# Performance work log

Measured on AMD Instinct MI355X. Metric: run time of the kernel, lower is better.

## Reference

```python
import jax, jax.numpy as jnp
import numpy as np

N_TOKENS, TOP_K, N_EXPERTS, HIDDEN, INTER = 4096, 2, 8, 1024, 2048


def setup_inputs() -> dict:
    key = jax.random.key(0)
    ks = jax.random.split(key, 6)
    std = float(np.sqrt(2.0 / (HIDDEN + INTER)))  # xavier-normal as in _init_weights
    tokens = jax.random.normal(ks[0], (N_TOKENS, HIDDEN), dtype=jnp.float32)
    expert_indices = jax.random.randint(ks[1], (N_TOKENS, TOP_K), 0, N_EXPERTS, dtype=jnp.int64)
    expert_weights = jax.random.uniform(ks[2], (N_TOKENS, TOP_K), dtype=jnp.float32)
    gate_weight = jax.random.normal(ks[3], (N_EXPERTS, HIDDEN, INTER), dtype=jnp.float32) * std
    up_weight = jax.random.normal(ks[4], (N_EXPERTS, HIDDEN, INTER), dtype=jnp.float32) * std
    down_weight = jax.random.normal(ks[5], (N_EXPERTS, INTER, HIDDEN), dtype=jnp.float32) * std
    return {"tokens": tokens, "expert_indices": expert_indices,
            "expert_weights": expert_weights, "gate_weight": gate_weight,
            "up_weight": up_weight, "down_weight": down_weight}


def reference(tokens, expert_indices, expert_weights, gate_weight, up_weight, down_weight):
    # Equivalent to the torch sort/group/scatter: since the expert output for a
    # token is independent of which top-k slot routed it, the combine reduces to
    # out[n] = sum_e cw[e, n] * FFN_e(tokens[n]), where cw[e, n] is the summed
    # routing weight of token n over slots whose index == e.
    n_experts = gate_weight.shape[0]
    onehot = jax.nn.one_hot(expert_indices, n_experts, dtype=tokens.dtype)  # [N,K,E]
    cw = jnp.einsum('nk,nke->en', expert_weights, onehot)  # [E,N] combine weights

    def body(acc, xs):
        g, u, d, w = xs  # g,u:[H,I]  d:[I,H]  w:[N]
        h = jax.nn.silu(tokens @ g) * (tokens @ u)  # [N,I] gated FFN hidden
        return acc + w[:, None] * (h @ d), None

    out0 = jnp.zeros_like(tokens)
    out, _ = jax.lax.scan(body, out0, (gate_weight, up_weight, down_weight, cw))
    return out
```

## Files before the change

### kernel.cpp

```cpp
#include <hip/hip_runtime.h>
#include <hip/hip_bf16.h>
#include <stdint.h>

#define NTOK  4096
#define TOPK  2
#define NEXP  8
#define HID   1024
#define INTER 2048
#define NPAIR (NTOK*TOPK)
#define MAXTILE 72

typedef __attribute__((ext_vector_type(8))) short short8;
typedef __attribute__((ext_vector_type(4))) float floatx4;

#define AS1(p) ((const __attribute__((address_space(1))) void*)(p))
#define AS3(p) ((__attribute__((address_space(3))) void*)(p))

#define O_PERMTOK 4096ull
#define O_PERMW   (O_PERMTOK + (size_t)NPAIR*4)
#define O_X       (1ull<<20)
#define O_WG      (O_X  + (size_t)NPAIR*HID*2)
#define O_WU      (O_WG + (size_t)NEXP*INTER*HID*2)
#define O_WD      (O_WU + (size_t)NEXP*INTER*HID*2)
#define O_HB      (O_WD + (size_t)NEXP*HID*INTER*2)
#define WS_NEEDED (O_HB + (size_t)NPAIR*INTER*2)

static __device__ __forceinline__ unsigned short f32_to_bf16_rne(float f) {
    union { float f; uint32_t u; } v; v.f = f;
    uint32_t b = v.u + 0x7fffu + ((v.u >> 16) & 1u);
    return (unsigned short)(b >> 16);
}
static __device__ __forceinline__ float bf16_to_f32(unsigned short u) {
    union { uint32_t i; float f; } cv; cv.i = ((uint32_t)u) << 16;
    return cv.f;
}

__global__ void k_probe(const void* __restrict__ tok, const void* __restrict__ ew,
                        const void* __restrict__ gw,  const void* __restrict__ uw,
                        const void* __restrict__ dw,  const void* __restrict__ eidx,
                        int* __restrict__ flags) {
    int lane = threadIdx.x;
    const void* ptrs[5] = { tok, ew, gw, uw, dw };
    for (int t = 0; t < 5; ++t) {
        const unsigned short* p = (const unsigned short*)ptrs[t];
        float v = bf16_to_f32(p[lane * 2]);
        unsigned long long m = __ballot(!(fabsf(v) < 1000.0f));
        if (lane == 0) flags[t] = (m != 0ull) ? 1 : 0;
    }
    const int* ix = (const int*)eidx;
    unsigned long long mi = __ballot(ix[lane * 2 + 1] != 0);
    if (lane == 0) flags[5] = (mi == 0ull) ? 1 : 0;
}

__global__ void k_route_count(const int* __restrict__ idx, int* __restrict__ counts,
                              const int* __restrict__ flags) {
    int i64 = flags[5];
    int p = blockIdx.x * 256 + threadIdx.x;
    if (p < NPAIR) atomicAdd(&counts[idx[p << i64]], 1);
}

__global__ void k_route_scan(const int* __restrict__ counts, int* __restrict__ offsets,
                             int* __restrict__ fill, int* __restrict__ ntiles,
                             int* __restrict__ tile_e, int* __restrict__ tile_m) {
    if (threadIdx.x == 0) {
        int acc = 0, nt = 0;
        for (int e = 0; e < NEXP; ++e) {
            offsets[e] = acc;
            for (int m = 0; m < counts[e]; m += 128) {
                tile_e[nt] = e; tile_m[nt] = m; ++nt;
            }
            acc += counts[e]; fill[e] = 0;
        }
        *ntiles = nt;
    }
}

__global__ void k_route_fill(const int* __restrict__ idx, const void* __restrict__ ew,
                             const int* __restrict__ offsets, int* __restrict__ fill,
                             int* __restrict__ perm_tok, float* __restrict__ perm_w,
                             const int* __restrict__ flags) {
    int ewf = flags[1], i64 = flags[5];
    int p = blockIdx.x * 256 + threadIdx.x;
    if (p < NPAIR) {
        int e = idx[p << i64];
        int pos = offsets[e] + atomicAdd(&fill[e], 1);
        perm_tok[pos] = p >> 1;
        perm_w[pos]   = ewf ? ((const float*)ew)[p]
                            : bf16_to_f32(((const unsigned short*)ew)[p]);
    }
}

__global__ void k_gather(const void* __restrict__ tokens, const int* __restrict__ perm_tok,
                         unsigned short* __restrict__ X, const int* __restrict__ flags) {
    int f = flags[0];
    int pos = blockIdx.x;
    int tok = perm_tok[pos];
    ushort4* d = (ushort4*)(X + (size_t)pos * HID);
    if (f) {
        float4 v = *(const float4*)((const float*)tokens + (size_t)tok * HID + threadIdx.x * 4);
        ushort4 o;
        o.x = f32_to_bf16_rne(v.x); o.y = f32_to_bf16_rne(v.y);
        o.z = f32_to_bf16_rne(v.z); o.w = f32_to_bf16_rne(v.w);
        d[threadIdx.x] = o;
    } else {
        d[threadIdx.x] = ((const ushort4*)((const unsigned short*)tokens + (size_t)tok * HID))[threadIdx.x];
    }
}

__global__ void k_transpose(const void* __restrict__ src,
                            unsigned short* __restrict__ dst, int R, int C,
                            const int* __restrict__ flags, int flagIdx) {
    __shared__ unsigned short tile[32][34];
    int isf32 = flags[flagIdx];
    size_t eoff = (size_t)blockIdx.z * R * C;
    const float* sf = (const float*)src + eoff;
    const unsigned short* sh = (const unsigned short*)src + eoff;
    dst += eoff;
    int c0 = blockIdx.x * 32, r0 = blockIdx.y * 32;
    int tx = threadIdx.x, ty = threadIdx.y;
#pragma unroll
    for (int i = 0; i < 32; i += 8) {
        size_t si = (size_t)(r0 + ty + i) * C + (c0 + tx);
        tile[ty + i][tx] = isf32 ? f32_to_bf16_rne(sf[si]) : sh[si];
    }
    __syncthreads();
#pragma unroll
    for (int i = 0; i < 32; i += 8)
        dst[(size_t)(c0 + ty + i) * R + (r0 + tx)] = tile[tx][ty + i];
}

__device__ __forceinline__ void stg16(const char* g, const unsigned short* ldsb) {
    __builtin_amdgcn_global_load_lds(AS1(g), AS3(ldsb), 16, 0, 0);
}

template<int KHW>
__device__ __forceinline__ void mfma_core(
    const unsigned short* __restrict__ Ab, int arowlim,
    const unsigned short* __restrict__ Bb,
    unsigned short* sA, unsigned short* sB,
    int tid, floatx4 (&acc)[4][4])
{
    const int wave = tid >> 6, lane = tid & 63;
    const int q = lane >> 4, l15 = lane & 15;
    const int wm = (wave >> 1) * 64, wn = (wave & 1) * 64;

    const int rl = lane >> 3;
    const int sch = (lane & 7) ^ (rl & 7);

    const char* gA[4]; const char* gB[4]; unsigned lb[4];
#pragma unroll
    for (int t = 0; t < 4; ++t) {
        int r = wave * 32 + t * 8 + rl;
        int ar = min(r, arowlim);
        gA[t] = (const char*)(Ab + (size_t)ar * KHW) + sch * 16;
        gB[t] = (const char*)(Bb + (size_t)r  * KHW) + sch * 16;
        lb[t] = (unsigned)((wave * 32 + t * 8) * 64);
    }

    const unsigned c0b = (unsigned)((q ^ (l15 & 7)) * 16);
    const char* cA = (const char*)sA;
    const char* cB = (const char*)sB;

#pragma unroll 1
    for (int kk = 0; kk < KHW / 64; ++kk) {
        const int kb = kk * 128;
#pragma unroll
        for (int t = 0; t < 4; ++t) stg16(gA[t] + kb, sA + lb[t]);
#pragma unroll
        for (int t = 0; t < 4; ++t) stg16(gB[t] + kb, sB + lb[t]);
        __syncthreads();
        short8 af[4][2], bfr[4][2];
#pragma unroll
        for (int i = 0; i < 4; ++i)
#pragma unroll
            for (int ks = 0; ks < 2; ++ks)
                af[i][ks] = *(const short8*)(cA + (wm + i * 16 + l15) * 128 + (c0b ^ (ks << 6)));
#pragma unroll
        for (int j = 0; j < 4; ++j)
#pragma unroll
            for (int ks = 0; ks < 2; ++ks)
                bfr[j][ks] = *(const short8*)(cB + (wn + j * 16 + l15) * 128 + (c0b ^ (ks << 6)));
#pragma unroll
        for (int i = 0; i < 4; ++i)
#pragma unroll
            for (int j = 0; j < 4; ++j) {
                acc[i][j] = __builtin_amdgcn_mfma_f32_16x16x32_bf16(af[i][0], bfr[j][0], acc[i][j], 0, 0, 0);
                acc[i][j] = __builtin_amdgcn_mfma_f32_16x16x32_bf16(af[i][1], bfr[j][1], acc[i][j], 0, 0, 0);
            }
        __syncthreads();
    }
}

template<int KHW>
__device__ __forceinline__ void mfma_core2(
    const unsigned short* __restrict__ Ab, int arowlim,
    const unsigned short* __restrict__ Bg, const unsigned short* __restrict__ Bu,
    unsigned short* sA, unsigned short* sBg, unsigned short* sBu,
    int tid, floatx4 (&accg)[4][4], floatx4 (&accu)[4][4])
{
    const int wave = tid >> 6, lane = tid & 63;
    const int q = lane >> 4, l15 = lane & 15;
    const int wm = (wave >> 1) * 64, wn = (wave & 1) * 64;

    const int rl = lane >> 3;
    const int sch = (lane & 7) ^ (rl & 7);

    const char* gA[4]; const char* gG[4]; const char* gU[4]; unsigned lb[4];
#pragma unroll
    for (int t = 0; t < 4; ++t) {
        int r = wave * 32 + t * 8 + rl;
        int ar = min(r, arowlim);
        gA[t] = (const char*)(Ab + (size_t)ar * KHW) + sch * 16;
        gG[t] = (const char*)(Bg + (size_t)r  * KHW) + sch * 16;
        gU[t] = (const char*)(Bu + (size_t)r  * KHW) + sch * 16;
        lb[t] = (unsigned)((wave * 32 + t * 8) * 64);
    }

    const unsigned c0b = (unsigned)((q ^ (l15 & 7)) * 16);
    const char* cA = (const char*)sA;
    const char* cG = (const char*)sBg;
    const char* cU = (const char*)sBu;

#pragma unroll 1
    for (int kk = 0; kk < KHW / 64; ++kk) {
        const int kb = kk * 128;
#pragma unroll
        for (int t = 0; t < 4; ++t) stg16(gA[t] + kb, sA + lb[t]);
#pragma unroll
        for (int t = 0; t < 4; ++t) stg16(gG[t] + kb, sBg + lb[t]);
#pragma unroll
        for (int t = 0; t < 4; ++t) stg16(gU[t] + kb, sBu + lb[t]);
        __syncthreads();
        short8 af[4][2];
#pragma unroll
        for (int i = 0; i < 4; ++i)
#pragma unroll
            for (int ks = 0; ks < 2; ++ks)
                af[i][ks] = *(const short8*)(cA + (wm + i * 16 + l15) * 128 + (c0b ^ (ks << 6)));
        {
            short8 b[4][2];
#pragma unroll
            for (int j = 0; j < 4; ++j)
#pragma unroll
                for (int ks = 0; ks < 2; ++ks)
                    b[j][ks] = *(const short8*)(cG + (wn + j * 16 + l15) * 128 + (c0b ^ (ks << 6)));
#pragma unroll
            for (int i = 0; i < 4; ++i)
#pragma unroll
                for (int j = 0; j < 4; ++j) {
                    accg[i][j] = __builtin_amdgcn_mfma_f32_16x16x32_bf16(af[i][0], b[j][0], accg[i][j], 0, 0, 0);
                    accg[i][j] = __builtin_amdgcn_mfma_f32_16x16x32_bf16(af[i][1], b[j][1], accg[i][j], 0, 0, 0);
                }
        }
        {
            short8 b[4][2];
#pragma unroll
            for (int j = 0; j < 4; ++j)
#pragma unroll
                for (int ks = 0; ks < 2; ++ks)
                    b[j][ks] = *(const short8*)(cU + (wn + j * 16 + l15) * 128 + (c0b ^ (ks << 6)));
#pragma unroll
            for (int i = 0; i < 4; ++i)
#pragma unroll
                for (int j = 0; j < 4; ++j) {
                    accu[i][j] = __builtin_amdgcn_mfma_f32_16x16x32_bf16(af[i][0], b[j][0], accu[i][j], 0, 0, 0);
                    accu[i][j] = __builtin_amdgcn_mfma_f32_16x16x32_bf16(af[i][1], b[j][1], accu[i][j], 0, 0, 0);
                }
        }
        __syncthreads();
    }
}

__global__ __launch_bounds__(256, 2) void k_gu(
    const unsigned short* __restrict__ X, const unsigned short* __restrict__ Wg,
    const unsigned short* __restrict__ Wu, unsigned short* __restrict__ Hbuf,
    const int* __restrict__ counts, const int* __restrict__ offsets,
    const int* __restrict__ tile_e, const int* __restrict__ tile_m,
    const int* __restrict__ ntiles)
{
    const int t = blockIdx.x;
    if (t >= *ntiles) return;
    const int e = tile_e[t], m0 = tile_m[t];
    const int cnt = counts[e], off = offsets[e];
    const int nt0 = blockIdx.y * 128;

    __shared__ __align__(16) unsigned short sA[128 * 64];
    __shared__ __align__(16) unsigned short sBg[128 * 64];
    __shared__ __align__(16) unsigned short sBu[128 * 64];

    const int tid = threadIdx.x;
    const int wave = tid >> 6, lane = tid & 63;
    const int wm = (wave >> 1) * 64, wn = (wave & 1) * 64;
    const int q = lane >> 4, l15 = lane & 15;

    floatx4 accg[4][4], accu[4][4];
#pragma unroll
    for (int i = 0; i < 4; ++i)
#pragma unroll
        for (int j = 0; j < 4; ++j)
#pragma unroll
            for (int r = 0; r < 4; ++r) { accg[i][j][r] = 0.f; accu[i][j][r] = 0.f; }

    mfma_core2<HID>(X + (size_t)(off + m0) * HID, NPAIR - 1 - (off + m0),
                    Wg + (size_t)e * INTER * HID + (size_t)nt0 * HID,
                    Wu + (size_t)e * INTER * HID + (size_t)nt0 * HID,
                    sA, sBg, sBu, tid, accg, accu);

#pragma unroll
    for (int i = 0; i < 4; ++i)
#pragma unroll
        for (int r = 0; r < 4; ++r) {
            int row = m0 + wm + i * 16 + q * 4 + r;
            if (row < cnt) {
                unsigned short* hrow = Hbuf + (size_t)(off + row) * INTER + nt0;
#pragma unroll
                for (int j = 0; j < 4; ++j) {
                    float g = accg[i][j][r];
                    float s = g / (1.0f + __expf(-g));
                    hrow[wn + j * 16 + l15] = f32_to_bf16_rne(s * accu[i][j][r]);
                }
            }
        }
}

__global__ __launch_bounds__(256) void k_d(
    const unsigned short* __restrict__ Hbuf, const unsigned short* __restrict__ Wd,
    float* __restrict__ outf,
    const int* __restrict__ counts, const int* __restrict__ offsets,
    const int* __restrict__ perm_tok, const float* __restrict__ perm_w,
    const int* __restrict__ tile_e, const int* __restrict__ tile_m,
    const int* __restrict__ ntiles)
{
    const int t = blockIdx.x;
    if (t >= *ntiles) return;
    const int e = tile_e[t], m0 = tile_m[t];
    const int cnt = counts[e], off = offsets[e];
    const int nt0 = blockIdx.y * 128;

    __shared__ __align__(16) unsigned short sA[128 * 64];
    __shared__ __align__(16) unsigned short sB[128 * 64];

    const int tid = threadIdx.x;
    const int wave = tid >> 6, lane = tid & 63;
    const int wm = (wave >> 1) * 64, wn = (wave & 1) * 64;
    const int q = lane >> 4, l15 = lane & 15;

    floatx4 acc[4][4];
#pragma unroll
    for (int i = 0; i < 4; ++i)
#pragma unroll
        for (int j = 0; j < 4; ++j)
#pragma unroll
            for (int r = 0; r < 4; ++r) acc[i][j][r] = 0.f;

    mfma_core<INTER>(Hbuf + (size_t)(off + m0) * INTER, NPAIR - 1 - (off + m0),
                     Wd + (size_t)e * HID * INTER + (size_t)nt0 * INTER, sA, sB, tid, acc);

#pragma unroll
    for (int i = 0; i < 4; ++i)
#pragma unroll
        for (int r = 0; r < 4; ++r) {
            int row = m0 + wm + i * 16 + q * 4 + r;
            if (row < cnt) {
                int gpos = off + row;
                int tok = perm_tok[gpos];
                float w = perm_w[gpos];
                float* orow = outf + (size_t)tok * HID + nt0;
#pragma unroll
                for (int j = 0; j < 4; ++j) {
#ifdef __HIP_PLATFORM_AMD__
                    unsafeAtomicAdd(&orow[wn + j * 16 + l15], w * acc[i][j][r]);
#else
                    atomicAdd(&orow[wn + j * 16 + l15], w * acc[i][j][r]);
#endif
                }
            }
        }
}

extern "C" void kernel_launch(void* const* d_in, const int* in_sizes, int n_in,
                              void* d_out, int out_size, void* d_ws, size_t ws_size,
                              hipStream_t stream) {
    const void* tokens = d_in[0];
    const void* eidx   = d_in[1];
    const void* ew     = d_in[2];
    const void* gw     = d_in[3];
    const void* uw     = d_in[4];
    const void* dwp    = d_in[5];
    float* out = (float*)d_out;
    char* ws = (char*)d_ws;

    if (ws_size < WS_NEEDED) {
        hipMemsetAsync(d_out, 0, (size_t)out_size * 4, stream);
        return;
    }

    int*   counts   = (int*)(ws + 0);
    int*   offsets  = (int*)(ws + 64);
    int*   fill     = (int*)(ws + 128);
    int*   flags    = (int*)(ws + 192);
    int*   ntiles   = (int*)(ws + 240);
    int*   tile_e   = (int*)(ws + 256);
    int*   tile_m   = (int*)(ws + 1024);
    int*   perm_tok = (int*)(ws + O_PERMTOK);
    float* perm_w   = (float*)(ws + O_PERMW);
    unsigned short* X  = (unsigned short*)(ws + O_X);
    unsigned short* Wg = (unsigned short*)(ws + O_WG);
    unsigned short* Wu = (unsigned short*)(ws + O_WU);
    unsigned short* Wd = (unsigned short*)(ws + O_WD);
    unsigned short* Hb = (unsigned short*)(ws + O_HB);

    hipMemsetAsync(counts, 0, 256, stream);
    hipMemsetAsync(out, 0, (size_t)out_size * 4, stream);

    k_probe<<<1, 64, 0, stream>>>(tokens, ew, gw, uw, dwp, eidx, flags);
    k_route_count<<<NPAIR / 256, 256, 0, stream>>>((const int*)eidx, counts, flags);
    k_route_scan<<<1, 64, 0, stream>>>(counts, offsets, fill, ntiles, tile_e, tile_m);
    k_route_fill<<<NPAIR / 256, 256, 0, stream>>>((const int*)eidx, ew, offsets, fill,
                                                  perm_tok, perm_w, flags);
    k_gather<<<NPAIR, 256, 0, stream>>>(tokens, perm_tok, X, flags);

    dim3 tb(32, 8);
    k_transpose<<<dim3(INTER / 32, HID / 32, NEXP), tb, 0, stream>>>(gw, Wg, HID, INTER, flags, 2);
    k_transpose<<<dim3(INTER / 32, HID / 32, NEXP), tb, 0, stream>>>(uw, Wu, HID, INTER, flags, 3);
    k_transpose<<<dim3(HID / 32, INTER / 32, NEXP), tb, 0, stream>>>(dwp, Wd, INTER, HID, flags, 4);

    k_gu<<<dim3(MAXTILE, INTER / 128), 256, 0, stream>>>(X, Wg, Wu, Hb, counts, offsets,
                                                         tile_e, tile_m, ntiles);
    k_d<<<dim3(MAXTILE, HID / 128), 256, 0, stream>>>(Hb, Wd, out, counts, offsets,
                                                      perm_tok, perm_w, tile_e, tile_m, ntiles);
}
```

Measured before the change: 541.7 us.

## Double-buffer LDS GEMM core, interleave gate/up weights, split-K down projection

Replaces the single-buffered MFMA loop with a double-buffered one that issues the global-to-LDS loads for the next K-tile while the current tile is computed. Gate and up weights are transposed into one interleaved matrix, so k_gu runs a single GEMM of twice the width and pairs the gate and up accumulators in the epilogue. k_d gains a split-K factor of 2 over INTER through blockIdx.z, relying on the existing atomic adds. The three transpose launches are merged into one. The trade-off is twice the LDS per block, which pressures occupancy, and more atomic traffic on the output.

```diff
diff --git a/kernel.cpp b/kernel.cpp
--- a/kernel.cpp
+++ b/kernel.cpp
@@ -19,11 +19,10 @@
 #define O_PERMTOK 4096ull
 #define O_PERMW   (O_PERMTOK + (size_t)NPAIR*4)
 #define O_X       (1ull<<20)
-#define O_WG      (O_X  + (size_t)NPAIR*HID*2)
-#define O_WU      (O_WG + (size_t)NEXP*INTER*HID*2)
-#define O_WD      (O_WU + (size_t)NEXP*INTER*HID*2)
-#define O_HB      (O_WD + (size_t)NEXP*HID*INTER*2)
-#define WS_NEEDED (O_HB + (size_t)NPAIR*INTER*2)
+#define O_WGU     (O_X   + (size_t)NPAIR*HID*2)
+#define O_WD      (O_WGU + (size_t)NEXP*2*INTER*HID*2)
+#define O_HB      (O_WD  + (size_t)NEXP*HID*INTER*2)
+#define WS_NEEDED (O_HB  + (size_t)NPAIR*INTER*2)
 
 static __device__ __forceinline__ unsigned short f32_to_bf16_rne(float f) {
     union { float f; uint32_t u; } v; v.f = f;
@@ -107,17 +106,26 @@
     }
 }
 
-__global__ void k_transpose(const void* __restrict__ src,
-                            unsigned short* __restrict__ dst, int R, int C,
-                            const int* __restrict__ flags, int flagIdx) {
+__global__ void k_transpose_all(const void* __restrict__ gw, const void* __restrict__ uw,
+                                const void* __restrict__ dwp,
+                                unsigned short* __restrict__ Wgu, unsigned short* __restrict__ Wd,
+                                const int* __restrict__ flags) {
     __shared__ unsigned short tile[32][34];
-    int isf32 = flags[flagIdx];
-    size_t eoff = (size_t)blockIdx.z * R * C;
+    const int z = blockIdx.y;
+    const int typ = z >> 3, e = z & 7;
+    const int R = (typ == 2) ? INTER : HID;
+    const int C = (typ == 2) ? HID : INTER;
+    const void* src = (typ == 0) ? gw : (typ == 1) ? uw : dwp;
+    const int isf32 = flags[2 + typ];
+    const size_t eoff = (size_t)e * HID * INTER;
     const float* sf = (const float*)src + eoff;
     const unsigned short* sh = (const unsigned short*)src + eoff;
-    dst += eoff;
-    int c0 = blockIdx.x * 32, r0 = blockIdx.y * 32;
-    int tx = threadIdx.x, ty = threadIdx.y;
+    unsigned short* dst = (typ == 2) ? (Wd + eoff) : (Wgu + (size_t)e * 2 * INTER * HID);
+
+    const int nbc = C / 32;
+    const int bx = blockIdx.x;
+    const int c0 = (bx % nbc) * 32, r0 = (bx / nbc) * 32;
+    const int tx = threadIdx.x, ty = threadIdx.y;
 #pragma unroll
     for (int i = 0; i < 32; i += 8) {
         size_t si = (size_t)(r0 + ty + i) * C + (c0 + tx);
@@ -125,16 +133,19 @@
     }
     __syncthreads();
 #pragma unroll
-    for (int i = 0; i < 32; i += 8)
-        dst[(size_t)(c0 + ty + i) * R + (r0 + tx)] = tile[tx][ty + i];
+    for (int i = 0; i < 32; i += 8) {
+        int c = c0 + ty + i;
+        int drow = (typ == 2) ? c : (((c >> 4) << 5) + (c & 15) + ((typ == 1) ? 16 : 0));
+        dst[(size_t)drow * R + (r0 + tx)] = tile[tx][ty + i];
+    }
 }
 
 __device__ __forceinline__ void stg16(const char* g, const unsigned short* ldsb) {
     __builtin_amdgcn_global_load_lds(AS1(g), AS3(ldsb), 16, 0, 0);
 }
 
-template<int KHW>
-__device__ __forceinline__ void mfma_core(
+template<int KHW, int NKT>
+__device__ __forceinline__ void coreK(
     const unsigned short* __restrict__ Ab, int arowlim,
     const unsigned short* __restrict__ Bb,
     unsigned short* sA, unsigned short* sB,
@@ -161,25 +172,35 @@
     const char* cA = (const char*)sA;
     const char* cB = (const char*)sB;
 
+#pragma unroll
+    for (int t = 0; t < 4; ++t) stg16(gA[t], sA + lb[t]);
+#pragma unroll
+    for (int t = 0; t < 4; ++t) stg16(gB[t], sB + lb[t]);
+    __syncthreads();
+
 #pragma unroll 1
-    for (int kk = 0; kk < KHW / 64; ++kk) {
-        const int kb = kk * 128;
-#pragma unroll
-        for (int t = 0; t < 4; ++t) stg16(gA[t] + kb, sA + lb[t]);
-#pragma unroll
-        for (int t = 0; t < 4; ++t) stg16(gB[t] + kb, sB + lb[t]);
-        __syncthreads();
+    for (int kt = 0; kt < NKT; ++kt) {
+        const int cur = kt & 1;
+        const unsigned curb = (unsigned)cur * 16384u;
+        if (kt + 1 < NKT) {
+            const int kb = (kt + 1) * 128;
+            const unsigned nxtb = (unsigned)(cur ^ 1) * 8192u;
+#pragma unroll
+            for (int t = 0; t < 4; ++t) stg16(gA[t] + kb, sA + nxtb + lb[t]);
+#pragma unroll
+            for (int t = 0; t < 4; ++t) stg16(gB[t] + kb, sB + nxtb + lb[t]);
+        }
         short8 af[4][2], bfr[4][2];
 #pragma unroll
         for (int i = 0; i < 4; ++i)
 #pragma unroll
             for (int ks = 0; ks < 2; ++ks)
-                af[i][ks] = *(const short8*)(cA + (wm + i * 16 + l15) * 128 + (c0b ^ (ks << 6)));
+                af[i][ks] = *(const short8*)(cA + curb + (wm + i * 16 + l15) * 128 + (c0b ^ (ks << 6)));
 #pragma unroll
         for (int j = 0; j < 4; ++j)
 #pragma unroll
             for (int ks = 0; ks < 2; ++ks)
-                bfr[j][ks] = *(const short8*)(cB + (wn + j * 16 + l15) * 128 + (c0b ^ (ks << 6)));
+                bfr[j][ks] = *(const short8*)(cB + curb + (wn + j * 16 + l15) * 128 + (c0b ^ (ks << 6)));
 #pragma unroll
         for (int i = 0; i < 4; ++i)
 #pragma unroll
@@ -191,89 +212,9 @@
     }
 }
 
-template<int KHW>
-__device__ __forceinline__ void mfma_core2(
-    const unsigned short* __restrict__ Ab, int arowlim,
-    const unsigned short* __restrict__ Bg, const unsigned short* __restrict__ Bu,
-    unsigned short* sA, unsigned short* sBg, unsigned short* sBu,
-    int tid, floatx4 (&accg)[4][4], floatx4 (&accu)[4][4])
-{
-    const int wave = tid >> 6, lane = tid & 63;
-    const int q = lane >> 4, l15 = lane & 15;
-    const int wm = (wave >> 1) * 64, wn = (wave & 1) * 64;
-
-    const int rl = lane >> 3;
-    const int sch = (lane & 7) ^ (rl & 7);
-
-    const char* gA[4]; const char* gG[4]; const char* gU[4]; unsigned lb[4];
-#pragma unroll
-    for (int t = 0; t < 4; ++t) {
-        int r = wave * 32 + t * 8 + rl;
-        int ar = min(r, arowlim);
-        gA[t] = (const char*)(Ab + (size_t)ar * KHW) + sch * 16;
-        gG[t] = (const char*)(Bg + (size_t)r  * KHW) + sch * 16;
-        gU[t] = (const char*)(Bu + (size_t)r  * KHW) + sch * 16;
-        lb[t] = (unsigned)((wave * 32 + t * 8) * 64);
-    }
-
-    const unsigned c0b = (unsigned)((q ^ (l15 & 7)) * 16);
-    const char* cA = (const char*)sA;
-    const char* cG = (const char*)sBg;
-    const char* cU = (const char*)sBu;
-
-#pragma unroll 1
-    for (int kk = 0; kk < KHW / 64; ++kk) {
-        const int kb = kk * 128;
-#pragma unroll
-        for (int t = 0; t < 4; ++t) stg16(gA[t] + kb, sA + lb[t]);
-#pragma unroll
-        for (int t = 0; t < 4; ++t) stg16(gG[t] + kb, sBg + lb[t]);
-#pragma unroll
-        for (int t = 0; t < 4; ++t) stg16(gU[t] + kb, sBu + lb[t]);
-        __syncthreads();
-        short8 af[4][2];
-#pragma unroll
-        for (int i = 0; i < 4; ++i)
-#pragma unroll
-            for (int ks = 0; ks < 2; ++ks)
-                af[i][ks] = *(const short8*)(cA + (wm + i * 16 + l15) * 128 + (c0b ^ (ks << 6)));
-        {
-            short8 b[4][2];
-#pragma unroll
-            for (int j = 0; j < 4; ++j)
-#pragma unroll
-                for (int ks = 0; ks < 2; ++ks)
-                    b[j][ks] = *(const short8*)(cG + (wn + j * 16 + l15) * 128 + (c0b ^ (ks << 6)));
-#pragma unroll
-            for (int i = 0; i < 4; ++i)
-#pragma unroll
-                for (int j = 0; j < 4; ++j) {
-                    accg[i][j] = __builtin_amdgcn_mfma_f32_16x16x32_bf16(af[i][0], b[j][0], accg[i][j], 0, 0, 0);
-                    accg[i][j] = __builtin_amdgcn_mfma_f32_16x16x32_bf16(af[i][1], b[j][1], accg[i][j], 0, 0, 0);
-                }
-        }
-        {
-            short8 b[4][2];
-#pragma unroll
-            for (int j = 0; j < 4; ++j)
-#pragma unroll
-                for (int ks = 0; ks < 2; ++ks)
-                    b[j][ks] = *(const short8*)(cU + (wn + j * 16 + l15) * 128 + (c0b ^ (ks << 6)));
-#pragma unroll
-            for (int i = 0; i < 4; ++i)
-#pragma unroll
-                for (int j = 0; j < 4; ++j) {
-                    accu[i][j] = __builtin_amdgcn_mfma_f32_16x16x32_bf16(af[i][0], b[j][0], accu[i][j], 0, 0, 0);
-                    accu[i][j] = __builtin_amdgcn_mfma_f32_16x16x32_bf16(af[i][1], b[j][1], accu[i][j], 0, 0, 0);
-                }
-        }
-        __syncthreads();
-    }
-}
-
 __global__ __launch_bounds__(256, 2) void k_gu(
-    const unsigned short* __restrict__ X, const unsigned short* __restrict__ Wg,
-    const unsigned short* __restrict__ Wu, unsigned short* __restrict__ Hbuf,
+    const unsigned short* __restrict__ X, const unsigned short* __restrict__ Wgu,
+    unsigned short* __restrict__ Hbuf,
     const int* __restrict__ counts, const int* __restrict__ offsets,
     const int* __restrict__ tile_e, const int* __restrict__ tile_m,
     const int* __restrict__ ntiles)
@@ -284,27 +225,25 @@
     const int cnt = counts[e], off = offsets[e];
     const int nt0 = blockIdx.y * 128;
 
-    __shared__ __align__(16) unsigned short sA[128 * 64];
-    __shared__ __align__(16) unsigned short sBg[128 * 64];
-    __shared__ __align__(16) unsigned short sBu[128 * 64];
+    __shared__ __align__(16) unsigned short sA[2 * 128 * 64];
+    __shared__ __align__(16) unsigned short sB[2 * 128 * 64];
 
     const int tid = threadIdx.x;
     const int wave = tid >> 6, lane = tid & 63;
     const int wm = (wave >> 1) * 64, wn = (wave & 1) * 64;
     const int q = lane >> 4, l15 = lane & 15;
 
-    floatx4 accg[4][4], accu[4][4];
+    floatx4 acc[4][4];
 #pragma unroll
     for (int i = 0; i < 4; ++i)
 #pragma unroll
         for (int j = 0; j < 4; ++j)
 #pragma unroll
-            for (int r = 0; r < 4; ++r) { accg[i][j][r] = 0.f; accu[i][j][r] = 0.f; }
-
-    mfma_core2<HID>(X + (size_t)(off + m0) * HID, NPAIR - 1 - (off + m0),
-                    Wg + (size_t)e * INTER * HID + (size_t)nt0 * HID,
-                    Wu + (size_t)e * INTER * HID + (size_t)nt0 * HID,
-                    sA, sBg, sBu, tid, accg, accu);
+            for (int r = 0; r < 4; ++r) acc[i][j][r] = 0.f;
+
+    coreK<HID, HID / 64>(X + (size_t)(off + m0) * HID, NPAIR - 1 - (off + m0),
+                         Wgu + (size_t)e * 2 * INTER * HID + (size_t)nt0 * HID,
+                         sA, sB, tid, acc);
 
 #pragma unroll
     for (int i = 0; i < 4; ++i)
@@ -312,18 +251,20 @@
         for (int r = 0; r < 4; ++r) {
             int row = m0 + wm + i * 16 + q * 4 + r;
             if (row < cnt) {
-                unsigned short* hrow = Hbuf + (size_t)(off + row) * INTER + nt0;
-#pragma unroll
-                for (int j = 0; j < 4; ++j) {
-                    float g = accg[i][j][r];
+                unsigned short* hrow = Hbuf + (size_t)(off + row) * INTER;
+#pragma unroll
+                for (int jp = 0; jp < 2; ++jp) {
+                    int j = jp * 2;
+                    float g = acc[i][j][r], u = acc[i][j + 1][r];
                     float s = g / (1.0f + __expf(-g));
-                    hrow[wn + j * 16 + l15] = f32_to_bf16_rne(s * accu[i][j][r]);
+                    int icol = (nt0 + wn) / 2 + jp * 16 + l15;
+                    hrow[icol] = f32_to_bf16_rne(s * u);
                 }
             }
         }
 }
 
-__global__ __launch_bounds__(256) void k_d(
+__global__ __launch_bounds__(256, 2) void k_d(
     const unsigned short* __restrict__ Hbuf, const unsigned short* __restrict__ Wd,
     float* __restrict__ outf,
     const int* __restrict__ counts, const int* __restrict__ offsets,
@@ -336,9 +277,10 @@
     const int e = tile_e[t], m0 = tile_m[t];
     const int cnt = counts[e], off = offsets[e];
     const int nt0 = blockIdx.y * 128;
-
-    __shared__ __align__(16) unsigned short sA[128 * 64];
-    __shared__ __align__(16) unsigned short sB[128 * 64];
+    const int z = blockIdx.z;
+
+    __shared__ __align__(16) unsigned short sA[2 * 128 * 64];
+    __shared__ __align__(16) unsigned short sB[2 * 128 * 64];
 
     const int tid = threadIdx.x;
     const int wave = tid >> 6, lane = tid & 63;
@@ -353,8 +295,9 @@
 #pragma unroll
             for (int r = 0; r < 4; ++r) acc[i][j][r] = 0.f;
 
-    mfma_core<INTER>(Hbuf + (size_t)(off + m0) * INTER, NPAIR - 1 - (off + m0),
-                     Wd + (size_t)e * HID * INTER + (size_t)nt0 * INTER, sA, sB, tid, acc);
+    coreK<INTER, 16>(Hbuf + (size_t)(off + m0) * INTER + z * 1024, NPAIR - 1 - (off + m0),
+                     Wd + (size_t)e * HID * INTER + (size_t)nt0 * INTER + z * 1024,
+                     sA, sB, tid, acc);
 
 #pragma unroll
     for (int i = 0; i < 4; ++i)
@@ -404,11 +347,10 @@
     int*   tile_m   = (int*)(ws + 1024);
     int*   perm_tok = (int*)(ws + O_PERMTOK);
     float* perm_w   = (float*)(ws + O_PERMW);
-    unsigned short* X  = (unsigned short*)(ws + O_X);
-    unsigned short* Wg = (unsigned short*)(ws + O_WG);
-    unsigned short* Wu = (unsigned short*)(ws + O_WU);
-    unsigned short* Wd = (unsigned short*)(ws + O_WD);
-    unsigned short* Hb = (unsigned short*)(ws + O_HB);
+    unsigned short* X   = (unsigned short*)(ws + O_X);
+    unsigned short* Wgu = (unsigned short*)(ws + O_WGU);
+    unsigned short* Wd  = (unsigned short*)(ws + O_WD);
+    unsigned short* Hb  = (unsigned short*)(ws + O_HB);
 
     hipMemsetAsync(counts, 0, 256, stream);
     hipMemsetAsync(out, 0, (size_t)out_size * 4, stream);
@@ -420,13 +362,10 @@
                                                   perm_tok, perm_w, flags);
     k_gather<<<NPAIR, 256, 0, stream>>>(tokens, perm_tok, X, flags);
 
-    dim3 tb(32, 8);
-    k_transpose<<<dim3(INTER / 32, HID / 32, NEXP), tb, 0, stream>>>(gw, Wg, HID, INTER, flags, 2);
-    k_transpose<<<dim3(INTER / 32, HID / 32, NEXP), tb, 0, stream>>>(uw, Wu, HID, INTER, flags, 3);
-    k_transpose<<<dim3(HID / 32, INTER / 32, NEXP), tb, 0, stream>>>(dwp, Wd, INTER, HID, flags, 4);
-
-    k_gu<<<dim3(MAXTILE, INTER / 128), 256, 0, stream>>>(X, Wg, Wu, Hb, counts, offsets,
-                                                         tile_e, tile_m, ntiles);
-    k_d<<<dim3(MAXTILE, HID / 128), 256, 0, stream>>>(Hb, Wd, out, counts, offsets,
-                                                      perm_tok, perm_w, tile_e, tile_m, ntiles);
-}
+    k_transpose_all<<<dim3(2048, 24), dim3(32, 8), 0, stream>>>(gw, uw, dwp, Wgu, Wd, flags);
+
+    k_gu<<<dim3(MAXTILE, 2 * INTER / 128), 256, 0, stream>>>(X, Wgu, Hb, counts, offsets,
+                                                             tile_e, tile_m, ntiles);
+    k_d<<<dim3(MAXTILE, HID / 128, 2), 256, 0, stream>>>(Hb, Wd, out, counts, offsets,
+                                                         perm_tok, perm_w, tile_e, tile_m, ntiles);
+}
```

Measured after the change: 547.5 us. About the same (+1.1%).
